# Kernel optimization log

Hardware: AMD Instinct MI355X
Metric: run time of the kernel (lower is better)

Reference implementation:

```python
import jax, jax.numpy as jnp
import numpy as np

B, S, D, H = 4, 2048, 768, 12
DK = D // H


def setup_inputs() -> dict:
    key = jax.random.key(0)
    ks = jax.random.split(key, 13)
    s = 1.0 / np.sqrt(D)
    inp = {
        "q": jax.random.normal(ks[0], (B, S, D), jnp.float32),
        "k": jax.random.normal(ks[1], (B, S, D), jnp.float32),
        "v": jax.random.normal(ks[2], (B, S, D), jnp.float32),
        "mask": jax.random.randint(ks[3], (B, S), 0, 2, jnp.int32),
        "Wq": jax.random.normal(ks[4], (D, D), jnp.float32) * s,
        "bq": jnp.zeros((D,), jnp.float32),
        "Wk": jax.random.normal(ks[5], (D, D), jnp.float32) * s,
        "bk": jnp.zeros((D,), jnp.float32),
        "Wv": jax.random.normal(ks[6], (D, D), jnp.float32) * s,
        "bv": jnp.zeros((D,), jnp.float32),
        "Wo": jax.random.normal(ks[7], (D, D), jnp.float32) * s,
        "bo": jnp.zeros((D,), jnp.float32),
    }
    return inp


def reference(q, k, v, mask, Wq, bq, Wk, bk, Wv, bv, Wo, bo):
    b, s, d = q.shape
    # projections (torch Linear: x @ W.T + b), split into heads: [b, h, s, dk]
    Q = (q @ Wq.T + bq).reshape(b, s, H, DK).transpose(0, 2, 1, 3)
    K = (k @ Wk.T + bk).reshape(b, s, H, DK).transpose(0, 2, 1, 3)
    V = (v @ Wv.T + bv).reshape(b, s, H, DK).transpose(0, 2, 1, 3)
    scores = jnp.einsum("bhqd,bhkd->bhqk", Q, K) / jnp.sqrt(jnp.float32(DK))
    # mask [b,s] -> [b,1,s,1]: masks whole query rows (faithful to source)
    scores = jnp.where(mask[:, None, :, None] == 0, jnp.float32(-1e9), scores)
    attn = jax.nn.softmax(scores, axis=-1)  # dropout is identity at inference
    out = jnp.einsum("bhqk,bhkd->bhqd", attn, V)
    concat = out.transpose(0, 2, 1, 3).reshape(b, s, d)
    return concat @ Wo.T + bo
```

## Files before the change

kernel.cpp:

```cpp
#include <hip/hip_runtime.h>

typedef _Float16 f16;
typedef f16 f16x2 __attribute__((ext_vector_type(2)));
typedef f16 f16x4 __attribute__((ext_vector_type(4)));
typedef f16 f16x8 __attribute__((ext_vector_type(8)));
typedef float f32x4 __attribute__((ext_vector_type(4)));
typedef float f32x16 __attribute__((ext_vector_type(16)));

#define B_ 4
#define S_ 2048
#define D_ 768
#define H_ 12
#define DK_ 64

__device__ __forceinline__ void dma16(const f16* g, f16* l) {
    __builtin_amdgcn_global_load_lds(
        (__attribute__((address_space(1))) void*)(uintptr_t)g,
        (__attribute__((address_space(3))) void*)l, 16, 0, 0);
}

__device__ __forceinline__ float exp2_raw(float x) {
#if __has_builtin(__builtin_amdgcn_exp2f)
    return __builtin_amdgcn_exp2f(x);
#else
    float r; asm("v_exp_f32 %0, %1" : "=v"(r) : "v"(x)); return r;
#endif
}

struct Cvt7 { const float* s[7]; f16* d[7]; };

__global__ __launch_bounds__(256) void cvt7_kernel(Cvt7 a)
{
    const int chunk = blockIdx.x * 256 + threadIdx.x;
    int z; int local;
    if (chunk < 2359296) { z = chunk / 786432; local = chunk - z * 786432; }
    else { int c2 = chunk - 2359296; int zi = c2 / 73728; z = 3 + zi; local = c2 - zi * 73728; }
    const size_t i = (size_t)local * 8;
    const float* __restrict__ s = a.s[z];
    float4 x = *(const float4*)(s + i);
    float4 y = *(const float4*)(s + i + 4);
    f16x8 h = {(f16)x.x, (f16)x.y, (f16)x.z, (f16)x.w,
               (f16)y.x, (f16)y.y, (f16)y.z, (f16)y.w};
    *(f16x8*)(a.d[z] + i) = h;
}

struct GemmArgs { const f16* A; const f16* W; const float* bias; float scale; void* C; int mode; };
struct GemmArgs3 { GemmArgs g[3]; };

template <int MODE>
__global__ __launch_bounds__(256, 4) void gemm_t(GemmArgs3 args)
{
    const int z = blockIdx.z;
    const f16* __restrict__ A = args.g[z].A;
    const f16* __restrict__ W = args.g[z].W;
    const float* __restrict__ bias = args.g[z].bias;
    const float scale = args.g[z].scale;

    __shared__ __align__(16) f16 As[128 * 64];
    __shared__ __align__(16) f16 Bs[128 * 64];

    const int tid = threadIdx.x, lane = tid & 63, w = tid >> 6;
    const int l15 = lane & 15, lg = lane >> 4;
    const int wm = (w >> 1) * 64, wn = (w & 1) * 64;
    const int m0 = blockIdx.y * 128, n0 = blockIdx.x * 128;

    const int lrow8 = lane >> 3;
    const int lchk8 = (lane & 7) ^ lrow8;
    const f16* gA = A + (size_t)(m0 + w * 32 + lrow8) * D_ + lchk8 * 8;
    const f16* gB = W + (size_t)(n0 + w * 32 + lrow8) * D_ + lchk8 * 8;

    f32x4 acc[4][4] = {};

    for (int kt = 0; kt < D_; kt += 64) {
        __syncthreads();
#pragma unroll
        for (int c = 0; c < 4; ++c) {
            dma16(gA + (size_t)(c * 8) * D_ + kt, &As[(w * 4 + c) * 512]);
            dma16(gB + (size_t)(c * 8) * D_ + kt, &Bs[(w * 4 + c) * 512]);
        }
        __syncthreads();
#pragma unroll
        for (int kk = 0; kk < 2; ++kk) {
            const int chk = ((kk * 4 + lg) ^ (l15 & 7)) * 8;
            f16x8 af[4], bf[4];
#pragma unroll
            for (int i = 0; i < 4; ++i)
                af[i] = *(const f16x8*)&As[(wm + i * 16 + l15) * 64 + chk];
#pragma unroll
            for (int j = 0; j < 4; ++j)
                bf[j] = *(const f16x8*)&Bs[(wn + j * 16 + l15) * 64 + chk];
#pragma unroll
            for (int i = 0; i < 4; ++i)
#pragma unroll
                for (int j = 0; j < 4; ++j)
                    acc[i][j] = __builtin_amdgcn_mfma_f32_16x16x32_f16(
                        bf[j], af[i], acc[i][j], 0, 0, 0);
        }
    }

    if constexpr (MODE == 0) {
        const int omode = args.g[z].mode;
        if (omode == 1) {
#pragma unroll
            for (int j = 0; j < 4; ++j) {
                int col = n0 + wn + j * 16 + lg * 4;
                float4 bb = *(const float4*)&bias[col];
#pragma unroll
                for (int i = 0; i < 4; ++i) {
                    int row = m0 + wm + i * 16 + l15;
                    int bI = row >> 11, sl = row & (S_ - 1);
                    f16* base = (f16*)args.g[z].C + (size_t)bI * D_ * S_ + sl;
                    base[(size_t)(col + 0) * S_] = (f16)(acc[i][j][0] + bb.x);
                    base[(size_t)(col + 1) * S_] = (f16)(acc[i][j][1] + bb.y);
                    base[(size_t)(col + 2) * S_] = (f16)(acc[i][j][2] + bb.z);
                    base[(size_t)(col + 3) * S_] = (f16)(acc[i][j][3] + bb.w);
                }
            }
        } else {
#pragma unroll
            for (int j = 0; j < 4; ++j) {
                int col = n0 + wn + j * 16 + lg * 4;
                float4 bb = *(const float4*)&bias[col];
#pragma unroll
                for (int i = 0; i < 4; ++i) {
                    int row = m0 + wm + i * 16 + l15;
                    f16x4 o = {(f16)((acc[i][j][0] + bb.x) * scale),
                               (f16)((acc[i][j][1] + bb.y) * scale),
                               (f16)((acc[i][j][2] + bb.z) * scale),
                               (f16)((acc[i][j][3] + bb.w) * scale)};
                    *(f16x4*)&((f16*)args.g[z].C)[(size_t)row * D_ + col] = o;
                }
            }
        }
    } else {
#pragma unroll
        for (int j = 0; j < 4; ++j) {
            int col = n0 + wn + j * 16 + lg * 4;
            float4 bb = *(const float4*)&bias[col];
#pragma unroll
            for (int i = 0; i < 4; ++i) {
                int row = m0 + wm + i * 16 + l15;
                float4 o = {acc[i][j][0] + bb.x, acc[i][j][1] + bb.y,
                            acc[i][j][2] + bb.z, acc[i][j][3] + bb.w};
                *(float4*)&((float*)args.g[z].C)[(size_t)row * D_ + col] = o;
            }
        }
    }
}

__global__ __launch_bounds__(256, 3) void attn_k(
    const f16* __restrict__ Qh, const f16* __restrict__ Kh,
    const f16* __restrict__ VhT, const int* __restrict__ mask,
    f16* __restrict__ O)
{
    __shared__ __align__(16) f16 lds[2][8192];
    const int tid = threadIdx.x, lane = tid & 63, w = tid >> 6;
    const int l31 = lane & 31, lhi = lane >> 5;

    const int bid = blockIdx.x;
    const int g8 = bid & 7, j5 = bid >> 3;
    const int head_lin = g8 * 6 + (j5 >> 4);
    const int qt = j5 & 15;
    const int b = head_lin / H_, h = head_lin % H_;
    const int q0 = qt * 128;
    const int rowbase = b * S_;
    const int col0 = h * DK_;

    const int lrow8 = lane >> 3;
    const int lchk8 = (lane & 7) ^ lrow8;

    {
        const f16* Qbase = Qh + (size_t)(rowbase + q0 + w * 32 + lrow8) * D_ + col0 + lchk8 * 8;
#pragma unroll
        for (int c = 0; c < 4; ++c)
            dma16(Qbase + (size_t)(c * 8) * D_, &lds[0][(w * 4 + c) * 512]);
    }
    __syncthreads();
    f16x8 qf[4];
    {
        const int qrow = w * 32 + l31;
        const f16 mf = (f16)((mask[rowbase + q0 + qrow] != 0) ? 1.0f : 0.0f);
#pragma unroll
        for (int dc = 0; dc < 4; ++dc) {
            f16x8 t = *(const f16x8*)&lds[0][qrow * 64 +
                                            (((dc * 2 + lhi) ^ (qrow & 7)) * 8)];
            qf[dc] = t * mf;
        }
    }
    __syncthreads();

    const f16* Kbase = Kh + (size_t)rowbase * D_ + col0;
    const f16* Vbase = VhT + ((size_t)b * D_ + col0) * S_;

#define STAGE(j)                                                              \
    {                                                                         \
        f16* Ksd = &lds[(j) & 1][0];                                          \
        f16* Vtd = &lds[(j) & 1][4096];                                       \
        const int k0s = (j) * 64;                                             \
        _Pragma("unroll")                                                     \
        for (int c = 0; c < 2; ++c) {                                         \
            int o = w * 2 + c;                                                \
            dma16(Kbase + (size_t)(k0s + o * 8 + lrow8) * D_ + lchk8 * 8,     \
                  &Ksd[o * 512]);                                             \
            dma16(Vbase + (size_t)(o * 8 + lrow8) * S_ + k0s + lchk8 * 8,     \
                  &Vtd[o * 512]);                                             \
        }                                                                     \
    }

    STAGE(0);
    STAGE(1);

    float rsum = 0.f;
    f32x16 acc[2] = {};

#pragma unroll 2
    for (int t = 0; t < 32; ++t) {
        const f16* Ksc = &lds[t & 1][0];
        const f16* Vtc = &lds[t & 1][4096];

        asm volatile("s_waitcnt vmcnt(4)" ::: "memory");
        __builtin_amdgcn_s_barrier();

#pragma unroll
        for (int kc = 0; kc < 2; ++kc) {
            f32x16 s = {};
            __builtin_amdgcn_s_setprio(1);
#pragma unroll
            for (int dc = 0; dc < 4; ++dc) {
                f16x8 kf = *(const f16x8*)&Ksc[(kc * 32 + l31) * 64 +
                                               (((dc * 2 + lhi) ^ (lane & 7)) * 8)];
                s = __builtin_amdgcn_mfma_f32_32x32x16_f16(kf, qf[dc], s, 0, 0, 0);
            }
            __builtin_amdgcn_s_setprio(0);
            f16x4 pb[4];
#pragma unroll
            for (int g = 0; g < 4; ++g) {
                float e0 = exp2_raw(s[4 * g + 0]);
                float e1 = exp2_raw(s[4 * g + 1]);
                float e2 = exp2_raw(s[4 * g + 2]);
                float e3 = exp2_raw(s[4 * g + 3]);
                rsum += (e0 + e1) + (e2 + e3);
                unsigned lo = __builtin_bit_cast(unsigned, __builtin_amdgcn_cvt_pkrtz(e0, e1));
                unsigned hi = __builtin_bit_cast(unsigned, __builtin_amdgcn_cvt_pkrtz(e2, e3));
                uint2 u; u.x = lo; u.y = hi;
                pb[g] = __builtin_bit_cast(f16x4, u);
            }
            __builtin_amdgcn_s_setprio(1);
#pragma unroll
            for (int g = 0; g < 4; ++g) {
                int kb = kc * 4 + g;
#pragma unroll
                for (int dc2 = 0; dc2 < 2; ++dc2) {
                    f16x4 vf = *(const f16x4*)&Vtc[(dc2 * 32 + l31) * 64 +
                                                   ((kb ^ (lane & 7)) * 8) + lhi * 4];
                    acc[dc2] = __builtin_amdgcn_mfma_f32_32x32x8f16(
                        vf, pb[g], acc[dc2], 0, 0, 0);
                }
            }
            __builtin_amdgcn_s_setprio(0);
        }

        asm volatile("s_waitcnt lgkmcnt(0)" ::: "memory");
        __builtin_amdgcn_s_barrier();
        if (t + 2 < 32) STAGE(t + 2);
    }

    rsum += __shfl_xor(rsum, 32, 64);
    const float inv = 1.0f / rsum;
    const size_t qrow = (size_t)(rowbase + q0 + w * 32 + l31);
#pragma unroll
    for (int dc2 = 0; dc2 < 2; ++dc2)
#pragma unroll
        for (int grp = 0; grp < 4; ++grp) {
            f16x4 ho = {(f16)(acc[dc2][4 * grp + 0] * inv),
                        (f16)(acc[dc2][4 * grp + 1] * inv),
                        (f16)(acc[dc2][4 * grp + 2] * inv),
                        (f16)(acc[dc2][4 * grp + 3] * inv)};
            *(f16x4*)&O[qrow * D_ + col0 + dc2 * 32 + grp * 8 + lhi * 4] = ho;
        }
#undef STAGE
}

extern "C" void kernel_launch(void* const* d_in, const int* in_sizes, int n_in,
                              void* d_out, int out_size, void* d_ws, size_t ws_size,
                              hipStream_t stream)
{
    const float* q    = (const float*)d_in[0];
    const float* k    = (const float*)d_in[1];
    const float* v    = (const float*)d_in[2];
    const int*   mask = (const int*)d_in[3];
    const float* Wq   = (const float*)d_in[4];
    const float* bq   = (const float*)d_in[5];
    const float* Wk   = (const float*)d_in[6];
    const float* bk   = (const float*)d_in[7];
    const float* Wv   = (const float*)d_in[8];
    const float* bv   = (const float*)d_in[9];
    const float* Wo   = (const float*)d_in[10];
    const float* bo   = (const float*)d_in[11];

    const size_t nQKV = (size_t)B_ * S_ * D_;
    const size_t nW   = (size_t)D_ * D_;

    f16* qh  = (f16*)d_ws;
    f16* kh  = qh + nQKV;
    f16* vh  = kh + nQKV;
    f16* Wqh = vh + nQKV;
    f16* Wkh = Wqh + nW;
    f16* Wvh = Wkh + nW;
    f16* Woh = Wvh + nW;
    f16* Qp  = Woh + nW;
    f16* Kp  = Qp + nQKV;
    f16* VpT = Kp + nQKV;
    f16* Cp  = VpT + nQKV;

    Cvt7 cv = {{q, k, v, Wq, Wk, Wv, Wo},
               {qh, kh, vh, Wqh, Wkh, Wvh, Woh}};
    cvt7_kernel<<<dim3(10368), 256, 0, stream>>>(cv);

    GemmArgs3 g1 = {{{qh, Wqh, bq, 1.44269504f / 8.0f, (void*)Qp, 0},
                     {kh, Wkh, bk, 1.0f, (void*)Kp, 0},
                     {vh, Wvh, bv, 1.0f, (void*)VpT, 1}}};
    gemm_t<0><<<dim3(6, 64, 3), 256, 0, stream>>>(g1);

    attn_k<<<dim3(768), 256, 0, stream>>>(Qp, Kp, VpT, mask, Cp);

    GemmArgs3 g2 = {{{Cp, Woh, bo, 1.0f, d_out, 2},
                     {Cp, Woh, bo, 1.0f, d_out, 2},
                     {Cp, Woh, bo, 1.0f, d_out, 2}}};
    gemm_t<2><<<dim3(6, 64, 1), 256, 0, stream>>>(g2);
}
```

Before: 283.9 us.

## Double-buffer GEMM LDS tiles with async DMA prefetch two stages ahead

Replaces the single-buffered load-sync-compute loop in the projection GEMM with a two-stage LDS ring, so the direct-to-LDS loads for tile t+2 are issued while tile t is being computed. Waits use vmcnt counters instead of full syncthreads. The last iteration of both the GEMM and the attention loop now waits on vmcnt(0). LDS use doubles, so launch bounds drop from 4 to 2 blocks per CU, which may reduce occupancy.

```diff
diff --git a/kernel.cpp b/kernel.cpp
--- a/kernel.cpp
+++ b/kernel.cpp
@@ -48,7 +48,7 @@
 struct GemmArgs3 { GemmArgs g[3]; };
 
 template <int MODE>
-__global__ __launch_bounds__(256, 4) void gemm_t(GemmArgs3 args)
+__global__ __launch_bounds__(256, 2) void gemm_t(GemmArgs3 args)
 {
     const int z = blockIdx.z;
     const f16* __restrict__ A = args.g[z].A;
@@ -56,8 +56,7 @@
     const float* __restrict__ bias = args.g[z].bias;
     const float scale = args.g[z].scale;
 
-    __shared__ __align__(16) f16 As[128 * 64];
-    __shared__ __align__(16) f16 Bs[128 * 64];
+    __shared__ __align__(16) f16 AB[2][2][8192];
 
     const int tid = threadIdx.x, lane = tid & 63, w = tid >> 6;
     const int l15 = lane & 15, lg = lane >> 4;
@@ -69,26 +68,42 @@
     const f16* gA = A + (size_t)(m0 + w * 32 + lrow8) * D_ + lchk8 * 8;
     const f16* gB = W + (size_t)(n0 + w * 32 + lrow8) * D_ + lchk8 * 8;
 
+#define GSTAGE(j)                                                             \
+    {                                                                         \
+        f16* Ad = &AB[(j) & 1][0][0];                                         \
+        f16* Bd = &AB[(j) & 1][1][0];                                         \
+        const int kts = (j) * 64;                                             \
+        _Pragma("unroll")                                                     \
+        for (int c = 0; c < 4; ++c) {                                         \
+            dma16(gA + (size_t)(c * 8) * D_ + kts, &Ad[(w * 4 + c) * 512]);   \
+            dma16(gB + (size_t)(c * 8) * D_ + kts, &Bd[(w * 4 + c) * 512]);   \
+        }                                                                     \
+    }
+
+    GSTAGE(0);
+    GSTAGE(1);
+
     f32x4 acc[4][4] = {};
 
-    for (int kt = 0; kt < D_; kt += 64) {
-        __syncthreads();
-#pragma unroll
-        for (int c = 0; c < 4; ++c) {
-            dma16(gA + (size_t)(c * 8) * D_ + kt, &As[(w * 4 + c) * 512]);
-            dma16(gB + (size_t)(c * 8) * D_ + kt, &Bs[(w * 4 + c) * 512]);
-        }
-        __syncthreads();
+#pragma unroll 2
+    for (int t = 0; t < 12; ++t) {
+        const f16* Asc = &AB[t & 1][0][0];
+        const f16* Bsc = &AB[t & 1][1][0];
+
+        if (t == 11) asm volatile("s_waitcnt vmcnt(0)" ::: "memory");
+        else         asm volatile("s_waitcnt vmcnt(8)" ::: "memory");
+        __builtin_amdgcn_s_barrier();
+
 #pragma unroll
         for (int kk = 0; kk < 2; ++kk) {
             const int chk = ((kk * 4 + lg) ^ (l15 & 7)) * 8;
             f16x8 af[4], bf[4];
 #pragma unroll
             for (int i = 0; i < 4; ++i)
-                af[i] = *(const f16x8*)&As[(wm + i * 16 + l15) * 64 + chk];
+                af[i] = *(const f16x8*)&Asc[(wm + i * 16 + l15) * 64 + chk];
 #pragma unroll
             for (int j = 0; j < 4; ++j)
-                bf[j] = *(const f16x8*)&Bs[(wn + j * 16 + l15) * 64 + chk];
+                bf[j] = *(const f16x8*)&Bsc[(wn + j * 16 + l15) * 64 + chk];
 #pragma unroll
             for (int i = 0; i < 4; ++i)
 #pragma unroll
@@ -96,7 +111,12 @@
                     acc[i][j] = __builtin_amdgcn_mfma_f32_16x16x32_f16(
                         bf[j], af[i], acc[i][j], 0, 0, 0);
         }
-    }
+
+        asm volatile("s_waitcnt lgkmcnt(0)" ::: "memory");
+        __builtin_amdgcn_s_barrier();
+        if (t + 2 < 12) GSTAGE(t + 2);
+    }
+#undef GSTAGE
 
     if constexpr (MODE == 0) {
         const int omode = args.g[z].mode;
@@ -218,7 +238,8 @@
         const f16* Ksc = &lds[t & 1][0];
         const f16* Vtc = &lds[t & 1][4096];
 
-        asm volatile("s_waitcnt vmcnt(4)" ::: "memory");
+        if (t == 31) asm volatile("s_waitcnt vmcnt(0)" ::: "memory");
+        else         asm volatile("s_waitcnt vmcnt(4)" ::: "memory");
         __builtin_amdgcn_s_barrier();
 
 #pragma unroll
```

Result: faster. 274.2 us (-3.4%).
